# Kernel tuning notes

Measured on AMD Instinct MI355X. Metric: run time of the kernel, lower is better.

The kernel has to match this reference:

```python
import jax, jax.numpy as jnp
import numpy as np

MAX_NUM_LEVELS = 3.5
NUM_LEVELS = 4  # mip levels 0..3 (levels clamped to [0, 2.5])


def affine_grid(matrix, N, H, W):
    # F.affine_grid, align_corners=False. matrix: (N,2,3) -> grid (N,H,W,2) in xy order.
    xs = (jnp.arange(W, dtype=jnp.float32) + 0.5) * (2.0 / W) - 1.0
    ys = (jnp.arange(H, dtype=jnp.float32) + 0.5) * (2.0 / H) - 1.0
    gy, gx = jnp.meshgrid(ys, xs, indexing='ij')
    base = jnp.stack([gx, gy, jnp.ones_like(gx)], axis=-1)  # (H,W,3)
    return jnp.einsum('hwk,nik->nhwi', base, matrix)  # (N,H,W,2)


def grid_sample_border(img, grid):
    # bilinear grid_sample, padding_mode='border', align_corners=False
    N, C, H, W = img.shape
    x = (grid[..., 0] + 1.0) * (W / 2.0) - 0.5
    y = (grid[..., 1] + 1.0) * (H / 2.0) - 0.5
    x0 = jnp.floor(x); y0 = jnp.floor(y)
    tx = x - x0; ty = y - y0
    x0i = jnp.clip(x0.astype(jnp.int32), 0, W - 1)
    x1i = jnp.clip(x0.astype(jnp.int32) + 1, 0, W - 1)
    y0i = jnp.clip(y0.astype(jnp.int32), 0, H - 1)
    y1i = jnp.clip(y0.astype(jnp.int32) + 1, 0, H - 1)
    b = jnp.arange(N)[:, None, None]
    g = lambda yi, xi: img[b, :, yi, xi]  # (N,Ho,Wo,C) gather
    out = (g(y0i, x0i) * ((1 - tx) * (1 - ty))[..., None]
           + g(y0i, x1i) * (tx * (1 - ty))[..., None]
           + g(y1i, x0i) * ((1 - tx) * ty)[..., None]
           + g(y1i, x1i) * (tx * ty)[..., None])
    return jnp.transpose(out, (0, 3, 1, 2))  # (N,C,Ho,Wo)


def blur_downsample(x):
    N, C, H, W = x.shape
    k1 = jnp.array([1., 3., 3., 1.], dtype=x.dtype) / 8.0
    k = k1[:, None] * k1[None, :]
    xp = jnp.pad(x, ((0, 0), (0, 0), (1, 2), (1, 2)), mode='reflect')
    kernel = jnp.broadcast_to(k[None, None], (C, 1, 4, 4))
    return jax.lax.conv_general_dilated(xp, kernel, window_strides=(2, 2), padding='VALID',
                                        feature_group_count=C,
                                        dimension_numbers=('NCHW', 'OIHW', 'NCHW'))


def compute_levels(grid, H, W):
    # per-pixel mip LOD from local stretch of the sampling grid (in source pixel units)
    coords = (grid + 1.0) * 0.5 * jnp.array([W, H], dtype=grid.dtype)  # (N,Ho,Wo,2)
    dx = coords[:, :-1, 1:] - coords[:, :-1, :-1]
    dy = coords[:, 1:, :-1] - coords[:, :-1, :-1]
    scale = jnp.maximum(jnp.linalg.norm(dx, axis=-1), jnp.linalg.norm(dy, axis=-1))
    scale = jnp.pad(scale, ((0, 0), (0, 1), (0, 1)), mode='edge')  # (N,Ho,Wo)
    levels = jnp.log2(jnp.maximum(scale, 1.0))
    return jnp.clip(levels, 0.0, MAX_NUM_LEVELS - 1.0)


def mipmap_warp(img, grid):
    N, C, H, W = img.shape
    levels = compute_levels(grid, H, W)  # (N,Ho,Wo)
    pyr = [img]
    for _ in range(NUM_LEVELS - 1):
        pyr.append(blur_downsample(pyr[-1]))
    samples = jnp.stack([grid_sample_border(p, grid) for p in pyr], axis=0)  # (L,N,C,Ho,Wo)
    ls = jnp.arange(NUM_LEVELS, dtype=levels.dtype)[:, None, None, None]
    w = jnp.clip(1.0 - jnp.abs(levels[None] - ls), 0.0, 1.0)  # trilinear blend weights (L,N,Ho,Wo)
    return jnp.einsum('lnhw,lnchw->nchw', w, samples)


def setup_inputs() -> dict:
    key = jax.random.key(0)
    k1, k2, k3 = jax.random.split(key, 3)
    N, C, H, W, D = 64, 3, 256, 256, 512
    img = jax.random.normal(k1, (N, C, H, W), dtype=jnp.float32)
    features = jax.random.normal(k2, (N, D), dtype=jnp.float32)
    # learned head params (zero-init in torch; small random here so the warp is nontrivial)
    lin_w = jax.random.normal(k3, (4, D), dtype=jnp.float32) * 0.02
    lin_b = jnp.zeros((4,), dtype=jnp.float32)
    return {'img': img, 'features': features, 'lin_w': lin_w, 'lin_b': lin_b}


def reference(img, features, lin_w, lin_b):
    params = features @ lin_w.T + lin_b  # (N,4)
    rot = jnp.tanh(params[:, 0:1]) * jnp.pi
    scale = jnp.exp(params[:, 1:2])
    sx, sy = params[:, 2:3], params[:, 3:4]
    c, s = jnp.cos(rot), jnp.sin(rot)
    matrix = jnp.concatenate([scale * c, -scale * s, sx, scale * s, scale * c, sy], axis=1).reshape(-1, 2, 3)
    affine_params = jnp.concatenate([rot, scale, sx, sy], axis=1)
    N, C, H, W = img.shape
    grid = affine_grid(matrix, N, H, W)
    out = mipmap_warp(img, grid)
    return out, grid, matrix, affine_params
```

## Files before the change

kernel.cpp:

```cpp
#include <hip/hip_runtime.h>
#include <math.h>

#define N_B 64
#define C_CH 3
#define H_IMG 256
#define W_IMG 256
#define D_FEAT 512

#define OUT_OFF_GRID   12582912
#define OUT_OFF_MATRIX 20971520
#define OUT_OFF_AFFINE 20971904

__global__ void params_kernel(const float* __restrict__ features,
                              const float* __restrict__ lin_w,
                              const float* __restrict__ lin_b,
                              float* __restrict__ out_matrix,
                              float* __restrict__ out_affine,
                              float* __restrict__ ws_params)
{
    const int n = blockIdx.x;
    const int t = threadIdx.x;
    const float* f = features + n * D_FEAT;
    float f0 = f[t];
    float f1 = f[t + 256];
    float a0 = f0 * lin_w[0 * D_FEAT + t] + f1 * lin_w[0 * D_FEAT + t + 256];
    float a1 = f0 * lin_w[1 * D_FEAT + t] + f1 * lin_w[1 * D_FEAT + t + 256];
    float a2 = f0 * lin_w[2 * D_FEAT + t] + f1 * lin_w[2 * D_FEAT + t + 256];
    float a3 = f0 * lin_w[3 * D_FEAT + t] + f1 * lin_w[3 * D_FEAT + t + 256];

    __shared__ float red[4][256];
    red[0][t] = a0; red[1][t] = a1; red[2][t] = a2; red[3][t] = a3;
    __syncthreads();
    for (int s = 128; s > 0; s >>= 1) {
        if (t < s) {
            red[0][t] += red[0][t + s];
            red[1][t] += red[1][t + s];
            red[2][t] += red[2][t + s];
            red[3][t] += red[3][t + s];
        }
        __syncthreads();
    }
    if (t == 0) {
        float p0 = red[0][0] + lin_b[0];
        float p1 = red[1][0] + lin_b[1];
        float p2 = red[2][0] + lin_b[2];
        float p3 = red[3][0] + lin_b[3];
        float rot   = tanhf(p0) * 3.14159265358979323846f;
        float scale = expf(p1);
        float c = cosf(rot), s = sinf(rot);
        float m00 = scale * c, m01 = -scale * s, m02 = p2;
        float m10 = scale * s, m11 =  scale * c, m12 = p3;
        out_matrix[n * 6 + 0] = m00;
        out_matrix[n * 6 + 1] = m01;
        out_matrix[n * 6 + 2] = m02;
        out_matrix[n * 6 + 3] = m10;
        out_matrix[n * 6 + 4] = m11;
        out_matrix[n * 6 + 5] = m12;
        out_affine[n * 4 + 0] = rot;
        out_affine[n * 4 + 1] = scale;
        out_affine[n * 4 + 2] = p2;
        out_affine[n * 4 + 3] = p3;
        float lv = log2f(fmaxf(scale, 1.0f));
        lv = fminf(fmaxf(lv, 0.0f), 2.5f);
        ws_params[n * 8 + 0] = m00;
        ws_params[n * 8 + 1] = m01;
        ws_params[n * 8 + 2] = m02;
        ws_params[n * 8 + 3] = m10;
        ws_params[n * 8 + 4] = m11;
        ws_params[n * 8 + 5] = m12;
        ws_params[n * 8 + 6] = lv;
        ws_params[n * 8 + 7] = 0.0f;
    }
}

template<int Hs, int Ws>
__global__ void down_kernel(const float* __restrict__ src, float* __restrict__ dst)
{
    constexpr int Hd = Hs / 2, Wd = Ws / 2;
    constexpr int PAIRS = Wd / 2;

    const int idx = blockIdx.x * blockDim.x + threadIdx.x;
    const int t   = idx & (PAIRS - 1);
    const int i   = (idx / PAIRS) & (Hd - 1);
    const int nc  = idx / (PAIRS * Hd);

    const float* __restrict__ s = src + (size_t)nc * Hs * Ws;

    int r[4];
#pragma unroll
    for (int a = 0; a < 4; a++) {
        int q = 2 * i + a - 1;
        if (q < 0) q = -q;
        if (q >= Hs) q = 2 * Hs - 2 - q;
        r[a] = q;
    }
    const int c4 = 4 * t;
    const int li = (t > 0)         ? c4 - 1 : 1;
    const int ri = (t < PAIRS - 1) ? c4 + 4 : Ws - 2;

    const float k0 = 0.125f, k1 = 0.375f;
    const float kr[4] = {0.125f, 0.375f, 0.375f, 0.125f};

    float acc0 = 0.0f, acc1 = 0.0f;
#pragma unroll
    for (int a = 0; a < 4; a++) {
        const float* row = s + (size_t)r[a] * Ws;
        float4 v = *(const float4*)(row + c4);
        float L = row[li];
        float R = row[ri];
        float h0 = k0 * L   + k1 * v.x + k1 * v.y + k0 * v.z;
        float h1 = k0 * v.y + k1 * v.z + k1 * v.w + k0 * R;
        acc0 += kr[a] * h0;
        acc1 += kr[a] * h1;
    }
    float2* d2 = (float2*)(dst + (size_t)nc * Hd * Wd + (size_t)i * Wd);
    d2[t] = make_float2(acc0, acc1);
}

__device__ __forceinline__ void sample_level(const float* __restrict__ p, int n, int l,
                                             float X, float Y, float out[3])
{
    const int Wl = W_IMG >> l;
    const int Hl = H_IMG >> l;
    float x = (X + 1.0f) * (0.5f * (float)Wl) - 0.5f;
    float y = (Y + 1.0f) * (0.5f * (float)Hl) - 0.5f;
    float x0f = floorf(x), y0f = floorf(y);
    float tx = x - x0f, ty = y - y0f;
    int x0 = (int)x0f, y0 = (int)y0f;
    int x0i = min(max(x0,     0), Wl - 1);
    int x1i = min(max(x0 + 1, 0), Wl - 1);
    int y0i = min(max(y0,     0), Hl - 1);
    int y1i = min(max(y0 + 1, 0), Hl - 1);
    float w00 = (1.0f - tx) * (1.0f - ty);
    float w01 = tx * (1.0f - ty);
    float w10 = (1.0f - tx) * ty;
    float w11 = tx * ty;
    const float* base = p + (size_t)n * C_CH * Hl * Wl;
#pragma unroll
    for (int c = 0; c < C_CH; c++) {
        const float* pc = base + (size_t)c * Hl * Wl;
        out[c] = w00 * pc[y0i * Wl + x0i] + w01 * pc[y0i * Wl + x1i]
               + w10 * pc[y1i * Wl + x0i] + w11 * pc[y1i * Wl + x1i];
    }
}

__device__ __forceinline__ const float* lvl_ptr(int l, const float* img,
                                                const float* p1, const float* p2,
                                                const float* p3)
{
    return (l == 0) ? img : ((l == 1) ? p1 : ((l == 2) ? p2 : p3));
}

__global__ void warp_kernel(const float* __restrict__ img,
                            const float* __restrict__ pyr1,
                            const float* __restrict__ pyr2,
                            const float* __restrict__ pyr3,
                            const float* __restrict__ ws_params,
                            float* __restrict__ out,
                            float* __restrict__ gridOut)
{
    const int n = blockIdx.y;
    const int tile = blockIdx.x;
    const int w = ((tile & 7) << 5) + (threadIdx.x & 31);
    const int h = ((tile >> 3) << 3) + (threadIdx.x >> 5);

    const float* P = ws_params + n * 8;
    float m00 = P[0], m01 = P[1], m02 = P[2];
    float m10 = P[3], m11 = P[4], m12 = P[5];
    float lv  = P[6];

    float gx = ((float)w + 0.5f) * (2.0f / (float)W_IMG) - 1.0f;
    float gy = ((float)h + 0.5f) * (2.0f / (float)H_IMG) - 1.0f;
    float X = m00 * gx + m01 * gy + m02;
    float Y = m10 * gx + m11 * gy + m12;

    float2* g2 = (float2*)gridOut;
    g2[(size_t)(n * H_IMG + h) * W_IMG + w] = make_float2(X, Y);

    int   l0   = (int)lv;
    float frac = lv - (float)l0;

    float c0[3];
    sample_level(lvl_ptr(l0, img, pyr1, pyr2, pyr3), n, l0, X, Y, c0);

    float r0, r1, r2;
    if (frac > 0.0f) {
        float c1[3];
        sample_level(lvl_ptr(l0 + 1, img, pyr1, pyr2, pyr3), n, l0 + 1, X, Y, c1);
        float w0 = 1.0f - frac;
        r0 = w0 * c0[0] + frac * c1[0];
        r1 = w0 * c0[1] + frac * c1[1];
        r2 = w0 * c0[2] + frac * c1[2];
    } else {
        r0 = c0[0]; r1 = c0[1]; r2 = c0[2];
    }

    size_t base = ((size_t)(n * C_CH + 0) * H_IMG + h) * W_IMG + w;
    out[base]                             = r0;
    out[base + (size_t)H_IMG * W_IMG]     = r1;
    out[base + (size_t)2 * H_IMG * W_IMG] = r2;
}

extern "C" void kernel_launch(void* const* d_in, const int* in_sizes, int n_in,
                              void* d_out, int out_size, void* d_ws, size_t ws_size,
                              hipStream_t stream)
{
    const float* img      = (const float*)d_in[0];
    const float* features = (const float*)d_in[1];
    const float* lin_w    = (const float*)d_in[2];
    const float* lin_b    = (const float*)d_in[3];

    float* out        = (float*)d_out;
    float* gridOut    = out + OUT_OFF_GRID;
    float* out_matrix = out + OUT_OFF_MATRIX;
    float* out_affine = out + OUT_OFF_AFFINE;

    float* ws        = (float*)d_ws;
    float* ws_params = ws;
    float* pyr1 = ws + 1024;
    float* pyr2 = pyr1 + (size_t)N_B * C_CH * 128 * 128;
    float* pyr3 = pyr2 + (size_t)N_B * C_CH * 64 * 64;

    params_kernel<<<N_B, 256, 0, stream>>>(features, lin_w, lin_b,
                                           out_matrix, out_affine, ws_params);

    int t1 = N_B * C_CH * 128 * 64;
    down_kernel<256, 256><<<t1 / 256, 256, 0, stream>>>(img,  pyr1);
    int t2 = N_B * C_CH * 64 * 32;
    down_kernel<128, 128><<<t2 / 256, 256, 0, stream>>>(pyr1, pyr2);
    int t3 = N_B * C_CH * 32 * 16;
    down_kernel<64, 64><<<t3 / 256, 256, 0, stream>>>(pyr2, pyr3);

    warp_kernel<<<dim3(H_IMG * W_IMG / 256, N_B), 256, 0, stream>>>(
        img, pyr1, pyr2, pyr3, ws_params, out, gridOut);
}
```

Before: 198.4 us.

## Stage warp source footprint in LDS and widen downsample to four outputs per thread

The warp kernel now computes each 32x8 tile's bounding box in the source mip levels, loads that footprint cooperatively into shared memory one channel at a time, and does the bilinear taps from LDS. If the footprint is too large it falls back to direct global gathers. The downsample kernel also produces four outputs per thread using two float4 loads instead of two outputs per thread. This targets scattered global gather traffic, at the cost of extra barriers per channel, bounding-box math, and wasted loads when tiles are heavily rotated or scaled.

After: 231.4 us. +16.6%, slower.

```diff
diff --git a/kernel.cpp b/kernel.cpp
--- a/kernel.cpp
+++ b/kernel.cpp
@@ -10,6 +10,11 @@
 #define OUT_OFF_GRID   12582912
 #define OUT_OFF_MATRIX 20971520
 #define OUT_OFF_AFFINE 20971904
+
+#define L0_STRIDE 68
+#define L0_ROWS   68
+#define L1_STRIDE 40
+#define L1_ROWS   40
 
 __global__ void params_kernel(const float* __restrict__ features,
                               const float* __restrict__ lin_w,
@@ -77,12 +82,12 @@
 __global__ void down_kernel(const float* __restrict__ src, float* __restrict__ dst)
 {
     constexpr int Hd = Hs / 2, Wd = Ws / 2;
-    constexpr int PAIRS = Wd / 2;
+    constexpr int QUADS = Wd / 4;
 
     const int idx = blockIdx.x * blockDim.x + threadIdx.x;
-    const int t   = idx & (PAIRS - 1);
-    const int i   = (idx / PAIRS) & (Hd - 1);
-    const int nc  = idx / (PAIRS * Hd);
+    const int t   = idx & (QUADS - 1);
+    const int i   = (idx / QUADS) & (Hd - 1);
+    const int nc  = idx / (QUADS * Hd);
 
     const float* __restrict__ s = src + (size_t)nc * Hs * Ws;
 
@@ -94,31 +99,43 @@
         if (q >= Hs) q = 2 * Hs - 2 - q;
         r[a] = q;
     }
-    const int c4 = 4 * t;
-    const int li = (t > 0)         ? c4 - 1 : 1;
-    const int ri = (t < PAIRS - 1) ? c4 + 4 : Ws - 2;
+    const int c8 = 8 * t;
+    const int li = (t > 0)         ? c8 - 1 : 1;
+    const int ri = (t < QUADS - 1) ? c8 + 8 : Ws - 2;
 
     const float k0 = 0.125f, k1 = 0.375f;
     const float kr[4] = {0.125f, 0.375f, 0.375f, 0.125f};
 
-    float acc0 = 0.0f, acc1 = 0.0f;
+    float acc0 = 0.f, acc1 = 0.f, acc2 = 0.f, acc3 = 0.f;
 #pragma unroll
     for (int a = 0; a < 4; a++) {
         const float* row = s + (size_t)r[a] * Ws;
-        float4 v = *(const float4*)(row + c4);
+        float4 A = *(const float4*)(row + c8);
+        float4 B = *(const float4*)(row + c8 + 4);
         float L = row[li];
         float R = row[ri];
-        float h0 = k0 * L   + k1 * v.x + k1 * v.y + k0 * v.z;
-        float h1 = k0 * v.y + k1 * v.z + k1 * v.w + k0 * R;
+        float h0 = k0 * L   + k1 * A.x + k1 * A.y + k0 * A.z;
+        float h1 = k0 * A.y + k1 * A.z + k1 * A.w + k0 * B.x;
+        float h2 = k0 * A.w + k1 * B.x + k1 * B.y + k0 * B.z;
+        float h3 = k0 * B.y + k1 * B.z + k1 * B.w + k0 * R;
         acc0 += kr[a] * h0;
         acc1 += kr[a] * h1;
-    }
-    float2* d2 = (float2*)(dst + (size_t)nc * Hd * Wd + (size_t)i * Wd);
-    d2[t] = make_float2(acc0, acc1);
-}
-
-__device__ __forceinline__ void sample_level(const float* __restrict__ p, int n, int l,
-                                             float X, float Y, float out[3])
+        acc2 += kr[a] * h2;
+        acc3 += kr[a] * h3;
+    }
+    float4* d4 = (float4*)(dst + (size_t)nc * Hd * Wd + (size_t)i * Wd + 4 * t);
+    *d4 = make_float4(acc0, acc1, acc2, acc3);
+}
+
+__device__ __forceinline__ const float* lvl_ptr(int l, const float* img,
+                                                const float* p1, const float* p2,
+                                                const float* p3)
+{
+    return (l == 0) ? img : ((l == 1) ? p1 : ((l == 2) ? p2 : p3));
+}
+
+__device__ __forceinline__ void sample_level_direct(const float* __restrict__ p, int n, int l,
+                                                    float X, float Y, float out[3])
 {
     const int Wl = W_IMG >> l;
     const int Hl = H_IMG >> l;
@@ -144,11 +161,63 @@
     }
 }
 
-__device__ __forceinline__ const float* lvl_ptr(int l, const float* img,
-                                                const float* p1, const float* p2,
-                                                const float* p3)
-{
-    return (l == 0) ? img : ((l == 1) ? p1 : ((l == 2) ? p2 : p3));
+__device__ __forceinline__ void tile_bbox(int l, int w0, int h0,
+                                          float m00, float m01, float m02,
+                                          float m10, float m11, float m12,
+                                          int& bx0, int& by0, int& bw, int& bh)
+{
+    const int Wl = W_IMG >> l;
+    const int Hl = H_IMG >> l;
+    float gx0 = ((float)w0 + 0.5f)  * (2.0f / W_IMG) - 1.0f;
+    float gx1 = ((float)w0 + 31.5f) * (2.0f / W_IMG) - 1.0f;
+    float gy0 = ((float)h0 + 0.5f)  * (2.0f / H_IMG) - 1.0f;
+    float gy1 = ((float)h0 + 7.5f)  * (2.0f / H_IMG) - 1.0f;
+
+    float X00 = m00 * gx0 + m01 * gy0 + m02;
+    float X10 = m00 * gx1 + m01 * gy0 + m02;
+    float X01 = m00 * gx0 + m01 * gy1 + m02;
+    float X11 = m00 * gx1 + m01 * gy1 + m02;
+    float Y00 = m10 * gx0 + m11 * gy0 + m12;
+    float Y10 = m10 * gx1 + m11 * gy0 + m12;
+    float Y01 = m10 * gx0 + m11 * gy1 + m12;
+    float Y11 = m10 * gx1 + m11 * gy1 + m12;
+
+    float hw = 0.5f * (float)Wl, hh = 0.5f * (float)Hl;
+    float xmin = fminf(fminf(X00, X10), fminf(X01, X11)) * hw + hw - 0.5f;
+    float xmax = fmaxf(fmaxf(X00, X10), fmaxf(X01, X11)) * hw + hw - 0.5f;
+    float ymin = fminf(fminf(Y00, Y10), fminf(Y01, Y11)) * hh + hh - 0.5f;
+    float ymax = fmaxf(fmaxf(Y00, Y10), fmaxf(Y01, Y11)) * hh + hh - 0.5f;
+
+    int ix0 = min(max((int)floorf(xmin), 0), Wl - 1);
+    int ix1 = min(max((int)floorf(xmax) + 1, 0), Wl - 1);
+    int iy0 = min(max((int)floorf(ymin), 0), Hl - 1);
+    int iy1 = min(max((int)floorf(ymax) + 1, 0), Hl - 1);
+    bx0 = ix0; by0 = iy0; bw = ix1 - ix0 + 1; bh = iy1 - iy0 + 1;
+}
+
+__device__ __forceinline__ void tap_setup(int l, float X, float Y, int bx0, int by0,
+                                          int stride, int& i00, int& i01, int& i10, int& i11,
+                                          float& w00, float& w01, float& w10, float& w11)
+{
+    const int Wl = W_IMG >> l;
+    const int Hl = H_IMG >> l;
+    float x = (X + 1.0f) * (0.5f * (float)Wl) - 0.5f;
+    float y = (Y + 1.0f) * (0.5f * (float)Hl) - 0.5f;
+    float x0f = floorf(x), y0f = floorf(y);
+    float tx = x - x0f, ty = y - y0f;
+    int x0 = (int)x0f, y0 = (int)y0f;
+    int x0i = min(max(x0,     0), Wl - 1) - bx0;
+    int x1i = min(max(x0 + 1, 0), Wl - 1) - bx0;
+    int y0i = min(max(y0,     0), Hl - 1) - by0;
+    int y1i = min(max(y0 + 1, 0), Hl - 1) - by0;
+    i00 = y0i * stride + x0i;
+    i01 = y0i * stride + x1i;
+    i10 = y1i * stride + x0i;
+    i11 = y1i * stride + x1i;
+    w00 = (1.0f - tx) * (1.0f - ty);
+    w01 = tx * (1.0f - ty);
+    w10 = (1.0f - tx) * ty;
+    w11 = tx * ty;
 }
 
 __global__ void warp_kernel(const float* __restrict__ img,
@@ -159,10 +228,16 @@
                             float* __restrict__ out,
                             float* __restrict__ gridOut)
 {
+    __shared__ float lds0[L0_ROWS * L0_STRIDE];
+    __shared__ float lds1[L1_ROWS * L1_STRIDE];
+
     const int n = blockIdx.y;
     const int tile = blockIdx.x;
-    const int w = ((tile & 7) << 5) + (threadIdx.x & 31);
-    const int h = ((tile >> 3) << 3) + (threadIdx.x >> 5);
+    const int tid = threadIdx.x;
+    const int w0 = (tile & 7) << 5;
+    const int h0 = (tile >> 3) << 3;
+    const int w = w0 + (tid & 31);
+    const int h = h0 + (tid >> 5);
 
     const float* P = ws_params + n * 8;
     float m00 = P[0], m01 = P[1], m02 = P[2];
@@ -179,26 +254,88 @@
 
     int   l0   = (int)lv;
     float frac = lv - (float)l0;
-
-    float c0[3];
-    sample_level(lvl_ptr(l0, img, pyr1, pyr2, pyr3), n, l0, X, Y, c0);
-
-    float r0, r1, r2;
-    if (frac > 0.0f) {
-        float c1[3];
-        sample_level(lvl_ptr(l0 + 1, img, pyr1, pyr2, pyr3), n, l0 + 1, X, Y, c1);
-        float w0 = 1.0f - frac;
-        r0 = w0 * c0[0] + frac * c1[0];
-        r1 = w0 * c0[1] + frac * c1[1];
-        r2 = w0 * c0[2] + frac * c1[2];
-    } else {
-        r0 = c0[0]; r1 = c0[1]; r2 = c0[2];
-    }
-
-    size_t base = ((size_t)(n * C_CH + 0) * H_IMG + h) * W_IMG + w;
-    out[base]                             = r0;
-    out[base + (size_t)H_IMG * W_IMG]     = r1;
-    out[base + (size_t)2 * H_IMG * W_IMG] = r2;
+    const bool hasL1 = (frac > 0.0f);
+
+    int bx0_0, by0_0, bw_0, bh_0;
+    tile_bbox(l0, w0, h0, m00, m01, m02, m10, m11, m12, bx0_0, by0_0, bw_0, bh_0);
+    int bx0_1 = 0, by0_1 = 0, bw_1 = 1, bh_1 = 1;
+    if (hasL1)
+        tile_bbox(l0 + 1, w0, h0, m00, m01, m02, m10, m11, m12, bx0_1, by0_1, bw_1, bh_1);
+
+    bool ldsOK = (bw_0 <= L0_STRIDE) && (bh_0 <= L0_ROWS) &&
+                 (!hasL1 || ((bw_1 <= L1_STRIDE) && (bh_1 <= L1_ROWS)));
+
+    size_t obase = ((size_t)n * C_CH * H_IMG + h) * W_IMG + w;
+
+    if (!ldsOK) {
+        float c0[3];
+        sample_level_direct(lvl_ptr(l0, img, pyr1, pyr2, pyr3), n, l0, X, Y, c0);
+        float r0, r1, r2;
+        if (hasL1) {
+            float c1[3];
+            sample_level_direct(lvl_ptr(l0 + 1, img, pyr1, pyr2, pyr3), n, l0 + 1, X, Y, c1);
+            float wA = 1.0f - frac;
+            r0 = wA * c0[0] + frac * c1[0];
+            r1 = wA * c0[1] + frac * c1[1];
+            r2 = wA * c0[2] + frac * c1[2];
+        } else {
+            r0 = c0[0]; r1 = c0[1]; r2 = c0[2];
+        }
+        out[obase]                             = r0;
+        out[obase + (size_t)H_IMG * W_IMG]     = r1;
+        out[obase + (size_t)2 * H_IMG * W_IMG] = r2;
+        return;
+    }
+
+    int i00, i01, i10, i11;  float w00, w01, w10, w11;
+    tap_setup(l0, X, Y, bx0_0, by0_0, L0_STRIDE, i00, i01, i10, i11, w00, w01, w10, w11);
+    int j00 = 0, j01 = 0, j10 = 0, j11 = 0;  float u00 = 0, u01 = 0, u10 = 0, u11 = 0;
+    if (hasL1)
+        tap_setup(l0 + 1, X, Y, bx0_1, by0_1, L1_STRIDE, j00, j01, j10, j11, u00, u01, u10, u11);
+
+    const int Wl0 = W_IMG >> l0, Hl0 = H_IMG >> l0;
+    const int Wl1 = W_IMG >> (l0 + 1), Hl1 = H_IMG >> (l0 + 1);
+    const float* base0 = lvl_ptr(l0, img, pyr1, pyr2, pyr3) + (size_t)n * C_CH * Hl0 * Wl0;
+    const float* base1 = hasL1 ? lvl_ptr(l0 + 1, img, pyr1, pyr2, pyr3) + (size_t)n * C_CH * Hl1 * Wl1
+                               : base0;
+
+    const int lane = tid & 63;
+    const int rgrp = tid >> 6;
+
+    float res[3];
+#pragma unroll
+    for (int c = 0; c < C_CH; c++) {
+        {
+            const float* plane = base0 + (size_t)c * Hl0 * Wl0;
+            for (int r = rgrp; r < bh_0; r += 4) {
+                const float* srow = plane + (size_t)(by0_0 + r) * Wl0 + bx0_0;
+                float* lrow = lds0 + r * L0_STRIDE;
+                if (lane < bw_0)      lrow[lane]      = srow[lane];
+                if (lane + 64 < bw_0) lrow[lane + 64] = srow[lane + 64];
+            }
+        }
+        if (hasL1) {
+            const float* plane = base1 + (size_t)c * Hl1 * Wl1;
+            for (int r = rgrp; r < bh_1; r += 4) {
+                const float* srow = plane + (size_t)(by0_1 + r) * Wl1 + bx0_1;
+                float* lrow = lds1 + r * L1_STRIDE;
+                if (lane < bw_1) lrow[lane] = srow[lane];
+            }
+        }
+        __syncthreads();
+
+        float v = w00 * lds0[i00] + w01 * lds0[i01] + w10 * lds0[i10] + w11 * lds0[i11];
+        if (hasL1) {
+            float u = u00 * lds1[j00] + u01 * lds1[j01] + u10 * lds1[j10] + u11 * lds1[j11];
+            v = (1.0f - frac) * v + frac * u;
+        }
+        res[c] = v;
+        __syncthreads();
+    }
+
+    out[obase]                             = res[0];
+    out[obase + (size_t)H_IMG * W_IMG]     = res[1];
+    out[obase + (size_t)2 * H_IMG * W_IMG] = res[2];
 }
 
 extern "C" void kernel_launch(void* const* d_in, const int* in_sizes, int n_in,
@@ -224,11 +361,11 @@
     params_kernel<<<N_B, 256, 0, stream>>>(features, lin_w, lin_b,
                                            out_matrix, out_affine, ws_params);
 
-    int t1 = N_B * C_CH * 128 * 64;
+    int t1 = N_B * C_CH * 128 * 32;
     down_kernel<256, 256><<<t1 / 256, 256, 0, stream>>>(img,  pyr1);
-    int t2 = N_B * C_CH * 64 * 32;
+    int t2 = N_B * C_CH * 64 * 16;
     down_kernel<128, 128><<<t2 / 256, 256, 0, stream>>>(pyr1, pyr2);
-    int t3 = N_B * C_CH * 32 * 16;
+    int t3 = N_B * C_CH * 32 * 8;
     down_kernel<64, 64><<<t3 / 256, 256, 0, stream>>>(pyr2, pyr3);
 
     warp_kernel<<<dim3(H_IMG * W_IMG / 256, N_B), 256, 0, stream>>>(
```
